# Performance work log

Measured on AMD Instinct MI355X. Metric: run time of the kernel, lower is better.

## Reference

```python
import jax, jax.numpy as jnp
import numpy as np

N, H, E, P = 100000, 64, 1600000, 3


def setup_inputs() -> dict:
    key = jax.random.key(0)
    ks = jax.random.split(key, 12)
    h = jax.random.normal(ks[0], (N, H), dtype=jnp.float32)
    W = jax.random.normal(ks[1], (P, H, H), dtype=jnp.float32) * 0.1
    b = jnp.zeros((P, H), dtype=jnp.float32)
    a = jnp.full((P,), 0.25, dtype=jnp.float32)  # PReLU slopes (torch default init)
    fc_w = jax.random.normal(ks[2], (H, H), dtype=jnp.float32) * 0.1
    fc_b = jnp.zeros((H,), dtype=jnp.float32)
    att = jax.random.normal(ks[3], (H,), dtype=jnp.float32) * 0.1
    adj_vals = jax.random.uniform(ks[4], (E,), dtype=jnp.float32) * (1.0 / 16.0)
    row = jax.random.randint(ks[5], (E,), 0, N, dtype=jnp.int32)
    col = jax.random.randint(ks[6], (E,), 0, N, dtype=jnp.int32)
    mask1 = jax.random.randint(ks[7], (N,), 0, 2, dtype=jnp.int32).astype(bool)
    mask2 = jax.random.randint(ks[8], (N,), 0, 2, dtype=jnp.int32).astype(bool)
    return {"h": h, "W": W, "b": b, "a": a, "fc_w": fc_w, "fc_b": fc_b,
            "att": att, "adj_vals": adj_vals, "row": row, "col": col,
            "mask1": mask1, "mask2": mask2}


def reference(h, W, b, a, fc_w, fc_b, att, adj_vals, row, col, mask1, mask2):
    n = h.shape[0]

    def gcn_all(x):
        # P GCN layers (small fixed P): linear -> spmm(adj) -> +bias -> PReLU
        outs = []
        for p in range(W.shape[0]):
            fts = x @ W[p].T                                   # [N,H]
            msg = fts[col] * adj_vals[:, None]                  # [E,H] gather
            agg = jax.ops.segment_sum(msg, row, num_segments=n) # [N,H] scatter-add
            o = agg + b[p]
            outs.append(jnp.where(o > 0, o, a[p] * o))          # PReLU
        return jnp.stack(outs)                                  # [P,N,H]

    def attention(embeds):
        # sp_p = mean_n tanh(fc(embed_p)); beta = softmax_p(att . sp_p)
        s = jnp.tanh(jnp.einsum('pnh,kh->pnk', embeds, fc_w) + fc_b).mean(axis=1)  # [P,H]
        beta = jax.nn.softmax(s @ att, axis=0)                                      # [P]
        return jnp.einsum('pnh,p->nh', embeds, beta)                                # [N,H]

    h_masked = h * (~mask1)[:, None].astype(h.dtype)
    z_mp = attention(gcn_all(h_masked))       # encode with mask_ratio1
    z_mp2 = attention(gcn_all(h))             # encode with mask_ratio 0
    z_masked = z_mp * (~mask2)[:, None].astype(h.dtype)
    x_recon = attention(gcn_all(z_masked))    # decode
    return (z_mp, z_mp2, x_recon)
```

## Files before the change

### kernel.cpp

```cpp
#include <hip/hip_runtime.h>
#include <hip/hip_bf16.h>

typedef __hip_bfloat16 bf16;
typedef __attribute__((ext_vector_type(8))) short bf16x8;
typedef __attribute__((ext_vector_type(4))) float f32x4;


__device__ __forceinline__ short f2bf(float x) {
    unsigned u = __float_as_uint(x);
    unsigned r = (u + 0x7FFFu + ((u >> 16) & 1u)) >> 16;
    return (short)r;
}
__device__ __forceinline__ float bf2f(short s) {
    return __uint_as_float(((unsigned)(unsigned short)s) << 16);
}

__device__ __forceinline__ void split8(const float* __restrict__ p, bool ok, bf16x8& hi,
                                       bf16x8& lo) {
    float v[8];
    if (ok) {
        float4 x0 = ((const float4*)p)[0];
        float4 x1 = ((const float4*)p)[1];
        v[0] = x0.x; v[1] = x0.y; v[2] = x0.z; v[3] = x0.w;
        v[4] = x1.x; v[5] = x1.y; v[6] = x1.z; v[7] = x1.w;
    } else {
#pragma unroll
        for (int j = 0; j < 8; j++) v[j] = 0.f;
    }
#pragma unroll
    for (int j = 0; j < 8; j++) {
        short hb = f2bf(v[j]);
        hi[j] = hb;
        lo[j] = f2bf(v[j] - bf2f(hb));
    }
}

__device__ __forceinline__ float fast_tanh(float x) {
    x = fminf(fmaxf(x, -15.f), 15.f);
    float t = __expf(2.f * x);
    return __fdividef(t - 1.f, t + 1.f);
}

__device__ __forceinline__ void fma4(float4& acc, float v, const float4& x) {
    acc.x = fmaf(v, x.x, acc.x);
    acc.y = fmaf(v, x.y, acc.y);
    acc.z = fmaf(v, x.z, acc.z);
    acc.w = fmaf(v, x.w, acc.w);
}

__device__ __forceinline__ void red4(float4& a) {
    a.x += __shfl_xor(a.x, 16); a.y += __shfl_xor(a.y, 16);
    a.z += __shfl_xor(a.z, 16); a.w += __shfl_xor(a.w, 16);
    a.x += __shfl_xor(a.x, 32); a.y += __shfl_xor(a.y, 32);
    a.z += __shfl_xor(a.z, 32); a.w += __shfl_xor(a.w, 32);
}

__global__ __launch_bounds__(256) void forensic_kernel(const unsigned int* __restrict__ mask_w,
                                                       const unsigned int* __restrict__ idx_w,
                                                       int nw_mask, int nw_idx,
                                                       int* __restrict__ flags) {
    __shared__ int sm[6];
    int t = threadIdx.x;
    if (t < 6) sm[t] = 0;
    __syncthreads();
    int m_gt1 = 0, m_f32 = 0, m_f64 = 0, m_oddnz = 0, i_hi = 0, i_oddnz = 0;
    for (int i = t; i < nw_mask; i += 256) {
        unsigned int w = mask_w[i];
        if (w > 1u && w != 0x3F800000u && w != 0x3FF00000u) m_gt1++;
        if (w == 0x3F800000u) m_f32++;
        if ((i & 1) && w == 0x3FF00000u) m_f64++;
        if ((i & 1) && w != 0u) m_oddnz++;
    }
    for (int i = t; i < nw_idx; i += 256) {
        unsigned int v = idx_w[i];
        if (v >= 0x20000000u) i_hi++;
        if ((i & 1) && v != 0u) i_oddnz++;
    }
    atomicAdd(&sm[0], m_gt1);
    atomicAdd(&sm[1], m_f32);
    atomicAdd(&sm[2], m_f64);
    atomicAdd(&sm[3], m_oddnz);
    atomicAdd(&sm[4], i_hi);
    atomicAdd(&sm[5], i_oddnz);
    __syncthreads();
    if (t == 0) {
        int mmode;
        if (sm[1] > 50) mmode = 2;
        else if (sm[2] > 50) mmode = 4;
        else if (sm[0] > 50) mmode = 0;
        else if (sm[3] > 50) mmode = 1;
        else mmode = 3;
        int imode;
        if (sm[4] > (nw_idx * 3) / 4) imode = 2;
        else if (sm[4] > nw_idx / 4) imode = 4;
        else if (sm[5] > 50) imode = 1;
        else imode = 3;
        flags[0] = mmode;
        flags[1] = imode;
    }
}

__device__ __forceinline__ int fetch_idx(const void* p, int e, int mode) {
    switch (mode) {
        case 1: return ((const int*)p)[e];
        case 3: return (int)(((const long long*)p)[e]);
        case 2: return (int)(((const float*)p)[e]);
        default: return (int)(((const double*)p)[e]);
    }
}

__global__ __launch_bounds__(256) void conv_mask_kernel(const void* __restrict__ m,
                                                        const int* __restrict__ flags, int n,
                                                        unsigned char* __restrict__ out) {
    int mode = flags[0];
    int i = blockIdx.x * 256 + threadIdx.x;
    if (i >= n) return;
    bool v;
    switch (mode) {
        case 0: v = ((const unsigned char*)m)[i] != 0; break;
        case 1: v = ((const int*)m)[i] != 0; break;
        case 2: v = ((const float*)m)[i] != 0.f; break;
        case 3: v = ((const long long*)m)[i] != 0; break;
        default: v = ((const double*)m)[i] != 0.0; break;
    }
    out[i] = v ? 1 : 0;
}


__global__ __launch_bounds__(256) void bucket_hist(const void* __restrict__ row,
                                                   const int* __restrict__ flags, int e_cnt,
                                                   int n, int shift, int nb,
                                                   int* __restrict__ bcnt) {
    __shared__ int hist[2048];
    int t = threadIdx.x;
    for (int i = t; i < nb; i += 256) hist[i] = 0;
    __syncthreads();
    int imode = flags[1];
    for (int e = blockIdx.x * 256 + t; e < e_cnt; e += gridDim.x * 256) {
        int r = fetch_idx(row, e, imode);
        if ((unsigned)r < (unsigned)n) atomicAdd(&hist[r >> shift], 1);
    }
    __syncthreads();
    for (int i = t; i < nb; i += 256)
        if (hist[i]) atomicAdd(&bcnt[i], hist[i]);
}

__global__ __launch_bounds__(1024) void bucket_scan(int* __restrict__ bptr, int nb,
                                                    int* __restrict__ bcur, int n,
                                                    int* __restrict__ row_ptr) {
    __shared__ int sh[1024];
    int t = threadIdx.x;
    int i0 = t * 2, i1 = t * 2 + 1;
    int a = (i0 < nb) ? bptr[i0] : 0;
    int b = (i1 < nb) ? bptr[i1] : 0;
    int s = a + b;
    sh[t] = s;
    __syncthreads();
    for (int off = 1; off < 1024; off <<= 1) {
        int u = (t >= off) ? sh[t - off] : 0;
        __syncthreads();
        sh[t] += u;
        __syncthreads();
    }
    int base = sh[t] - s;
    if (i0 < nb) { bptr[i0] = base; bcur[i0] = base; }
    if (i1 < nb) { bptr[i1] = base + a; bcur[i1] = base + a; }
    if (t == 1023) {
        bptr[nb] = sh[1023];
        row_ptr[n] = sh[1023];
    }
}

__global__ __launch_bounds__(256) void bin_pass2(const void* __restrict__ row,
                                                 const void* __restrict__ col,
                                                 const float* __restrict__ vals,
                                                 const int* __restrict__ flags, int e_cnt, int n,
                                                 int shift, int nb, int epb,
                                                 int* __restrict__ bcur,
                                                 int2* __restrict__ rcbin,
                                                 float* __restrict__ valbin) {
    __shared__ int hist[2048];
    __shared__ int base[2048];
    int t = threadIdx.x;
    int e0 = blockIdx.x * epb;
    int e1 = e0 + epb;
    if (e1 > e_cnt) e1 = e_cnt;
    if (e0 >= e_cnt) return;
    int imode = flags[1];
    for (int i = t; i < nb; i += 256) hist[i] = 0;
    __syncthreads();
    for (int e = e0 + t; e < e1; e += 256) {
        int r = fetch_idx(row, e, imode);
        if ((unsigned)r < (unsigned)n) atomicAdd(&hist[r >> shift], 1);
    }
    __syncthreads();
    for (int i = t; i < nb; i += 256) {
        int c = hist[i];
        base[i] = c ? atomicAdd(&bcur[i], c) : 0;
        hist[i] = 0;
    }
    __syncthreads();
    for (int e = e0 + t; e < e1; e += 256) {
        int r = fetch_idx(row, e, imode);
        if ((unsigned)r >= (unsigned)n) continue;
        int c = fetch_idx(col, e, imode);
        if ((unsigned)c >= (unsigned)n) c = 0;
        int bk = r >> shift;
        int pos = base[bk] + atomicAdd(&hist[bk], 1);
        rcbin[pos] = make_int2(r, c);
        valbin[pos] = vals[e];
    }
}

__global__ __launch_bounds__(256) void csr_finalize(const int* __restrict__ bptr,
                                                    const int2* __restrict__ rcbin,
                                                    const float* __restrict__ valbin, int n,
                                                    int shift, int* __restrict__ row_ptr,
                                                    int* __restrict__ col_s,
                                                    float* __restrict__ val_s) {
    __shared__ int cnt[1024];
    __shared__ int curs[1024];
    __shared__ int red[256];
    int b = blockIdx.x, t = threadIdx.x;
    int rpb = 1 << shift;
    int r0 = b << shift;
    int rows = n - r0;
    if (rows <= 0) return;
    if (rows > rpb) rows = rpb;
    int ebase = bptr[b], eend = bptr[b + 1];
    for (int i = t; i < rows; i += 256) cnt[i] = 0;
    __syncthreads();
    for (int e = ebase + t; e < eend; e += 256) atomicAdd(&cnt[rcbin[e].x - r0], 1);
    __syncthreads();
    int v[4], s = 0;
#pragma unroll
    for (int j = 0; j < 4; j++) {
        int idx = t * 4 + j;
        v[j] = (idx < rows) ? cnt[idx] : 0;
        s += v[j];
    }
    red[t] = s;
    __syncthreads();
    for (int off = 1; off < 256; off <<= 1) {
        int u = (t >= off) ? red[t - off] : 0;
        __syncthreads();
        red[t] += u;
        __syncthreads();
    }
    int run = ebase + red[t] - s;
#pragma unroll
    for (int j = 0; j < 4; j++) {
        int idx = t * 4 + j;
        if (idx < rows) {
            row_ptr[r0 + idx] = run;
            curs[idx] = run;
            run += v[j];
        }
    }
    __syncthreads();
    for (int e = ebase + t; e < eend; e += 256) {
        int2 rc = rcbin[e];
        float vv = valbin[e];
        int pos = atomicAdd(&curs[rc.x - r0], 1);
        col_s[pos] = rc.y;
        val_s[pos] = vv;
    }
}


__global__ __launch_bounds__(256) void spmm_dual(const float* __restrict__ X,
                                                 const int* __restrict__ row_ptr,
                                                 const int* __restrict__ col_s,
                                                 const float* __restrict__ val_s,
                                                 const unsigned char* __restrict__ mask, int n,
                                                 float* __restrict__ ax_m,
                                                 float* __restrict__ ax_f) {
    int gid = blockIdx.x * 256 + threadIdx.x;
    int r = gid >> 6;
    if (r >= n) return;
    int lane = threadIdx.x & 63;
    int g = lane >> 4, sub = lane & 15;
    int s = row_ptr[r], e = row_ptr[r + 1];
    int cnt = e - s;
    int myc = 0;
    float myvf = 0.f, myvm = 0.f;
    if (lane < cnt) {
        myc = col_s[s + lane];
        float v = val_s[s + lane];
        myvf = v;
        myvm = mask[myc] ? 0.f : v;
    }
    int cmain = cnt > 64 ? 64 : cnt;
    float4 fA = {0, 0, 0, 0}, fB = {0, 0, 0, 0}, mA = {0, 0, 0, 0}, mB = {0, 0, 0, 0};
    for (int i = 0; i < cmain; i += 8) {
        int iA = i + g, iB = i + 4 + g;
        int cA = __shfl(myc, iA), cB = __shfl(myc, iB);
        float vfA = __shfl(myvf, iA), vfB = __shfl(myvf, iB);
        float vmA = __shfl(myvm, iA), vmB = __shfl(myvm, iB);
        if (iA < cmain) {
            float4 x = *(const float4*)(X + (size_t)cA * 64 + sub * 4);
            fma4(fA, vfA, x);
            fma4(mA, vmA, x);
        }
        if (iB < cmain) {
            float4 x = *(const float4*)(X + (size_t)cB * 64 + sub * 4);
            fma4(fB, vfB, x);
            fma4(mB, vmB, x);
        }
    }
    for (int i = 64 + g; i < cnt; i += 4) {
        int c = col_s[s + i];
        float v = val_s[s + i];
        float vm = mask[c] ? 0.f : v;
        float4 x = *(const float4*)(X + (size_t)c * 64 + sub * 4);
        fma4(fA, v, x);
        fma4(mA, vm, x);
    }
    fA.x += fB.x; fA.y += fB.y; fA.z += fB.z; fA.w += fB.w;
    mA.x += mB.x; mA.y += mB.y; mA.z += mB.z; mA.w += mB.w;
    red4(fA);
    red4(mA);
    if (g == 0) {
        *(float4*)(ax_f + (size_t)r * 64 + sub * 4) = fA;
        *(float4*)(ax_m + (size_t)r * 64 + sub * 4) = mA;
    }
}

__global__ __launch_bounds__(256) void spmm_one(const float* __restrict__ X,
                                                const int* __restrict__ row_ptr,
                                                const int* __restrict__ col_s,
                                                const float* __restrict__ val_s,
                                                const unsigned char* __restrict__ mask, int n,
                                                float* __restrict__ ax) {
    int gid = blockIdx.x * 256 + threadIdx.x;
    int r = gid >> 6;
    if (r >= n) return;
    int lane = threadIdx.x & 63;
    int g = lane >> 4, sub = lane & 15;
    int s = row_ptr[r], e = row_ptr[r + 1];
    int cnt = e - s;
    int myc = 0;
    float myv = 0.f;
    if (lane < cnt) {
        myc = col_s[s + lane];
        float v = val_s[s + lane];
        myv = mask[myc] ? 0.f : v;
    }
    int cmain = cnt > 64 ? 64 : cnt;
    float4 aA = {0, 0, 0, 0}, aB = {0, 0, 0, 0};
    for (int i = 0; i < cmain; i += 8) {
        int iA = i + g, iB = i + 4 + g;
        int cA = __shfl(myc, iA), cB = __shfl(myc, iB);
        float vA = __shfl(myv, iA), vB = __shfl(myv, iB);
        if (iA < cmain && vA != 0.f) {
            float4 x = *(const float4*)(X + (size_t)cA * 64 + sub * 4);
            fma4(aA, vA, x);
        }
        if (iB < cmain && vB != 0.f) {
            float4 x = *(const float4*)(X + (size_t)cB * 64 + sub * 4);
            fma4(aB, vB, x);
        }
    }
    for (int i = 64 + g; i < cnt; i += 4) {
        int c = col_s[s + i];
        if (mask[c]) continue;
        float v = val_s[s + i];
        float4 x = *(const float4*)(X + (size_t)c * 64 + sub * 4);
        fma4(aA, v, x);
    }
    aA.x += aB.x; aA.y += aB.y; aA.z += aB.z; aA.w += aB.w;
    red4(aA);
    if (g == 0) *(float4*)(ax + (size_t)r * 64 + sub * 4) = aA;
}


template <int PP>
__global__ __launch_bounds__(256) void gemm_tanh(const float* __restrict__ X,
                                                 const float* __restrict__ Wg,
                                                 const float* __restrict__ b,
                                                 const float* __restrict__ a,
                                                 const float* __restrict__ fcw,
                                                 const float* __restrict__ fcb, int n,
                                                 float* __restrict__ s_sums) {
    __shared__ __align__(16) float tile[PP][16][68];
    int t = threadIdx.x;
    int wv = t >> 6, lane = t & 63, nl = lane & 15, q = lane >> 4;
    int colg = wv * 16 + nl;
    bf16x8 whi[PP][2], wlo[PP][2];
    float bias[PP], slope[PP];
#pragma unroll
    for (int p = 0; p < PP; p++) {
#pragma unroll
        for (int kk = 0; kk < 2; kk++)
            split8(Wg + p * 4096 + colg * 64 + kk * 32 + q * 8, true, whi[p][kk], wlo[p][kk]);
        bias[p] = b[p * 64 + colg];
        slope[p] = a[p];
    }
    bf16x8 fhi[2], flo[2];
#pragma unroll
    for (int kk = 0; kk < 2; kk++)
        split8(fcw + colg * 64 + kk * 32 + q * 8, true, fhi[kk], flo[kk]);
    float fbias = fcb[colg];
    float ssum[PP];
#pragma unroll
    for (int p = 0; p < PP; p++) ssum[p] = 0.f;

    int ntiles = (n + 15) >> 4;
    for (int rt = blockIdx.x; rt < ntiles; rt += gridDim.x) {
        int rowi = rt * 16 + nl;
        bool ok = rowi < n;
        bf16x8 ah[2], al[2];
#pragma unroll
        for (int kk = 0; kk < 2; kk++)
            split8(X + (size_t)rowi * 64 + kk * 32 + q * 8, ok, ah[kk], al[kk]);
#pragma unroll
        for (int p = 0; p < PP; p++) {
            f32x4 acc = {0.f, 0.f, 0.f, 0.f};
            acc = __builtin_amdgcn_mfma_f32_16x16x32_bf16(ah[0], whi[p][0], acc, 0, 0, 0);
            acc = __builtin_amdgcn_mfma_f32_16x16x32_bf16(ah[1], whi[p][1], acc, 0, 0, 0);
            acc = __builtin_amdgcn_mfma_f32_16x16x32_bf16(al[0], whi[p][0], acc, 0, 0, 0);
            acc = __builtin_amdgcn_mfma_f32_16x16x32_bf16(al[1], whi[p][1], acc, 0, 0, 0);
            acc = __builtin_amdgcn_mfma_f32_16x16x32_bf16(ah[0], wlo[p][0], acc, 0, 0, 0);
            acc = __builtin_amdgcn_mfma_f32_16x16x32_bf16(ah[1], wlo[p][1], acc, 0, 0, 0);
            acc = __builtin_amdgcn_mfma_f32_16x16x32_bf16(al[0], wlo[p][0], acc, 0, 0, 0);
            acc = __builtin_amdgcn_mfma_f32_16x16x32_bf16(al[1], wlo[p][1], acc, 0, 0, 0);
#pragma unroll
            for (int i = 0; i < 4; i++) {
                float o = acc[i] + bias[p];
                tile[p][q * 4 + i][colg] = (o > 0.f) ? o : slope[p] * o;
            }
        }
        __syncthreads();
#pragma unroll
        for (int p = 0; p < PP; p++) {
            bf16x8 eh[2], el[2];
#pragma unroll
            for (int kk = 0; kk < 2; kk++)
                split8(&tile[p][nl][kk * 32 + q * 8], true, eh[kk], el[kk]);
            f32x4 acc = {0.f, 0.f, 0.f, 0.f};
            acc = __builtin_amdgcn_mfma_f32_16x16x32_bf16(eh[0], fhi[0], acc, 0, 0, 0);
            acc = __builtin_amdgcn_mfma_f32_16x16x32_bf16(eh[1], fhi[1], acc, 0, 0, 0);
            acc = __builtin_amdgcn_mfma_f32_16x16x32_bf16(el[0], fhi[0], acc, 0, 0, 0);
            acc = __builtin_amdgcn_mfma_f32_16x16x32_bf16(el[1], fhi[1], acc, 0, 0, 0);
            acc = __builtin_amdgcn_mfma_f32_16x16x32_bf16(eh[0], flo[0], acc, 0, 0, 0);
            acc = __builtin_amdgcn_mfma_f32_16x16x32_bf16(eh[1], flo[1], acc, 0, 0, 0);
#pragma unroll
            for (int i = 0; i < 4; i++) {
                int r = rt * 16 + q * 4 + i;
                if (r < n) ssum[p] += fast_tanh(acc[i] + fbias);
            }
        }
        __syncthreads();
    }
#pragma unroll
    for (int p = 0; p < PP; p++) {
        float s = ssum[p];
        s += __shfl_xor(s, 16);
        s += __shfl_xor(s, 32);
        if (q == 0) atomicAdd(&s_sums[p * 64 + colg], s);
    }
}


template <int PP>
__global__ __launch_bounds__(256) void gemm_mix(const float* __restrict__ X,
                                                const float* __restrict__ Wg,
                                                const float* __restrict__ b,
                                                const float* __restrict__ a,
                                                const float* __restrict__ beta, int n,
                                                float* __restrict__ out, int accum) {
    int t = threadIdx.x;
    int wv = t >> 6, lane = t & 63, nl = lane & 15, q = lane >> 4;
    int colg = wv * 16 + nl;
    bf16x8 whi[PP][2], wlo[PP][2];
    float bias[PP], slope[PP], bet[PP];
#pragma unroll
    for (int p = 0; p < PP; p++) {
#pragma unroll
        for (int kk = 0; kk < 2; kk++)
            split8(Wg + p * 4096 + colg * 64 + kk * 32 + q * 8, true, whi[p][kk], wlo[p][kk]);
        bias[p] = b[p * 64 + colg];
        slope[p] = a[p];
        bet[p] = beta[p];
    }
    int ntiles = (n + 15) >> 4;
    for (int rt = blockIdx.x; rt < ntiles; rt += gridDim.x) {
        int rowi = rt * 16 + nl;
        bool ok = rowi < n;
        bf16x8 ah[2], al[2];
#pragma unroll
        for (int kk = 0; kk < 2; kk++)
            split8(X + (size_t)rowi * 64 + kk * 32 + q * 8, ok, ah[kk], al[kk]);
        float mix[4] = {0.f, 0.f, 0.f, 0.f};
#pragma unroll
        for (int p = 0; p < PP; p++) {
            f32x4 acc = {0.f, 0.f, 0.f, 0.f};
            acc = __builtin_amdgcn_mfma_f32_16x16x32_bf16(ah[0], whi[p][0], acc, 0, 0, 0);
            acc = __builtin_amdgcn_mfma_f32_16x16x32_bf16(ah[1], whi[p][1], acc, 0, 0, 0);
            acc = __builtin_amdgcn_mfma_f32_16x16x32_bf16(al[0], whi[p][0], acc, 0, 0, 0);
            acc = __builtin_amdgcn_mfma_f32_16x16x32_bf16(al[1], whi[p][1], acc, 0, 0, 0);
            acc = __builtin_amdgcn_mfma_f32_16x16x32_bf16(ah[0], wlo[p][0], acc, 0, 0, 0);
            acc = __builtin_amdgcn_mfma_f32_16x16x32_bf16(ah[1], wlo[p][1], acc, 0, 0, 0);
            acc = __builtin_amdgcn_mfma_f32_16x16x32_bf16(al[0], wlo[p][0], acc, 0, 0, 0);
            acc = __builtin_amdgcn_mfma_f32_16x16x32_bf16(al[1], wlo[p][1], acc, 0, 0, 0);
#pragma unroll
            for (int i = 0; i < 4; i++) {
                float o = acc[i] + bias[p];
                o = (o > 0.f) ? o : slope[p] * o;
                mix[i] = fmaf(bet[p], o, mix[i]);
            }
        }
#pragma unroll
        for (int i = 0; i < 4; i++) {
            int r = rt * 16 + q * 4 + i;
            if (r < n) {
                size_t idx = (size_t)r * 64 + colg;
                out[idx] = accum ? (out[idx] + mix[i]) : mix[i];
            }
        }
    }
}

__global__ __launch_bounds__(64) void compute_beta(const float* __restrict__ s_sums,
                                                   const float* __restrict__ att, int n, int P,
                                                   float* __restrict__ beta) {
    int lane = threadIdx.x;
    float av = att[lane];
    float l[8];
    for (int p = 0; p < P; p++) l[p] = s_sums[p * 64 + lane] * av;
#pragma unroll
    for (int off = 32; off > 0; off >>= 1)
        for (int p = 0; p < 8; p++)
            if (p < P) l[p] += __shfl_down(l[p], off);
    if (lane == 0) {
        const float inv = 1.0f / (float)n;
        float m = -1e30f;
        for (int p = 0; p < P; p++) {
            l[p] *= inv;
            m = fmaxf(m, l[p]);
        }
        float s = 0.f;
        for (int p = 0; p < P; p++) {
            l[p] = __expf(l[p] - m);
            s += l[p];
        }
        for (int p = 0; p < P; p++) beta[p] = l[p] / s;
    }
}


extern "C" void kernel_launch(void* const* d_in, const int* in_sizes, int n_in,
                              void* d_out, int out_size, void* d_ws, size_t ws_size,
                              hipStream_t stream) {
    const float* h = (const float*)d_in[0];
    const float* W = (const float*)d_in[1];
    const float* b = (const float*)d_in[2];
    const float* a = (const float*)d_in[3];
    const float* fc_w = (const float*)d_in[4];
    const float* fc_b = (const float*)d_in[5];
    const float* att = (const float*)d_in[6];
    const float* adj = (const float*)d_in[7];
    const void* row = d_in[8];
    const void* col = d_in[9];
    const void* mask1 = d_in[10];
    const void* mask2 = d_in[11];
    float* out = (float*)d_out;

    int P = in_sizes[3];
    if (P < 1 || P > 8) P = 3;
    int N = in_sizes[0] / 64;
    int E = in_sizes[7];

    int shift = 8;
    while (((N >> shift) + 1) > 2048) shift++;
    int NB = (N >> shift) + 1;

    char* w = (char*)d_ws;
    auto alloc = [&](size_t bytes) {
        void* p = (void*)w;
        w += (bytes + 255) & ~(size_t)255;
        return p;
    };
    int* row_ptr = (int*)alloc((size_t)(N + 1) * 4);
    int* col_s = (int*)alloc((size_t)E * 4);
    float* val_s = (float*)alloc((size_t)E * 4);
    int* bptr = (int*)alloc((size_t)(NB + 1) * 4);
    int* bcur = (int*)alloc((size_t)NB * 4);
    int2* rcbin = (int2*)alloc((size_t)E * 8);
    float* valbin = (float*)alloc((size_t)E * 4);
    unsigned char* m1c = (unsigned char*)alloc(N);
    unsigned char* m2c = (unsigned char*)alloc(N);
    float* axm = (float*)alloc((size_t)N * 64 * 4);
    float* axf = (float*)alloc((size_t)N * 64 * 4);
    float* s_sums = (float*)alloc(8 * 64 * 4);
    float* beta = (float*)alloc(8 * 4);
    int* flags = (int*)alloc(256);

    int nw_mask = N / 4 > 25000 ? 25000 : N / 4;
    int nw_idx = E / 4 > 25000 ? 25000 : E / 4;
    forensic_kernel<<<1, 256, 0, stream>>>((const unsigned int*)mask1, (const unsigned int*)row,
                                           nw_mask, nw_idx, flags);
    conv_mask_kernel<<<(N + 255) / 256, 256, 0, stream>>>(mask1, flags, N, m1c);
    conv_mask_kernel<<<(N + 255) / 256, 256, 0, stream>>>(mask2, flags, N, m2c);

    hipMemsetAsync(bptr, 0, (size_t)(NB + 1) * 4, stream);
    bucket_hist<<<1024, 256, 0, stream>>>(row, flags, E, N, shift, NB, bptr);
    bucket_scan<<<1, 1024, 0, stream>>>(bptr, NB, bcur, N, row_ptr);
    int epb = 8192;
    int bin_blocks = (E + epb - 1) / epb;
    bin_pass2<<<bin_blocks, 256, 0, stream>>>(row, col, adj, flags, E, N, shift, NB, epb, bcur,
                                              rcbin, valbin);
    csr_finalize<<<NB, 256, 0, stream>>>(bptr, rcbin, valbin, N, shift, row_ptr, col_s, val_s);

    int spmm_grid = ((size_t)N * 64 + 255) / 256;
    int gemm_blocks = 1024;

    auto tail = [&](const float* ax, float* dst) {
        hipMemsetAsync(s_sums, 0, 8 * 64 * 4, stream);
        if (P == 3) {
            gemm_tanh<3><<<gemm_blocks, 256, 0, stream>>>(ax, W, b, a, fc_w, fc_b, N, s_sums);
        } else {
            for (int p = 0; p < P; p++)
                gemm_tanh<1><<<gemm_blocks, 256, 0, stream>>>(ax, W + p * 4096, b + p * 64, a + p,
                                                              fc_w, fc_b, N, s_sums + p * 64);
        }
        compute_beta<<<1, 64, 0, stream>>>(s_sums, att, N, P, beta);
        if (P == 3) {
            gemm_mix<3><<<gemm_blocks, 256, 0, stream>>>(ax, W, b, a, beta, N, dst, 0);
        } else {
            for (int p = 0; p < P; p++)
                gemm_mix<1><<<gemm_blocks, 256, 0, stream>>>(ax, W + p * 4096, b + p * 64, a + p,
                                                             beta + p, N, dst, p != 0);
        }
    };

    spmm_dual<<<spmm_grid, 256, 0, stream>>>(h, row_ptr, col_s, val_s, m1c, N, axm, axf);
    tail(axm, out);
    tail(axf, out + (size_t)N * 64);
    spmm_one<<<spmm_grid, 256, 0, stream>>>(out, row_ptr, col_s, val_s, m2c, N, axm);
    tail(axm, out + (size_t)2 * N * 64);
}
```

Measured before the change: 655.7 us.

## Fuse mask conversion, register-cache bin pass, widen finalize and spmm unroll

Result: no change. 652.8 us (-0.4%).

```diff
diff --git a/kernel.cpp b/kernel.cpp
--- a/kernel.cpp
+++ b/kernel.cpp
@@ -109,21 +109,26 @@
     }
 }
 
-__global__ __launch_bounds__(256) void conv_mask_kernel(const void* __restrict__ m,
-                                                        const int* __restrict__ flags, int n,
-                                                        unsigned char* __restrict__ out) {
+__device__ __forceinline__ bool conv_one(const void* m, int mode, int i) {
+    switch (mode) {
+        case 0: return ((const unsigned char*)m)[i] != 0;
+        case 1: return ((const int*)m)[i] != 0;
+        case 2: return ((const float*)m)[i] != 0.f;
+        case 3: return ((const long long*)m)[i] != 0;
+        default: return ((const double*)m)[i] != 0.0;
+    }
+}
+
+__global__ __launch_bounds__(256) void conv_masks(const void* __restrict__ m1,
+                                                  const void* __restrict__ m2,
+                                                  const int* __restrict__ flags, int n,
+                                                  unsigned char* __restrict__ o1,
+                                                  unsigned char* __restrict__ o2) {
     int mode = flags[0];
     int i = blockIdx.x * 256 + threadIdx.x;
     if (i >= n) return;
-    bool v;
-    switch (mode) {
-        case 0: v = ((const unsigned char*)m)[i] != 0; break;
-        case 1: v = ((const int*)m)[i] != 0; break;
-        case 2: v = ((const float*)m)[i] != 0.f; break;
-        case 3: v = ((const long long*)m)[i] != 0; break;
-        default: v = ((const double*)m)[i] != 0.0; break;
-    }
-    out[i] = v ? 1 : 0;
+    o1[i] = conv_one(m1, mode, i) ? 1 : 0;
+    o2[i] = conv_one(m2, mode, i) ? 1 : 0;
 }
 
 
@@ -175,23 +180,35 @@
                                                  const void* __restrict__ col,
                                                  const float* __restrict__ vals,
                                                  const int* __restrict__ flags, int e_cnt, int n,
-                                                 int shift, int nb, int epb,
-                                                 int* __restrict__ bcur,
+                                                 int shift, int nb, int* __restrict__ bcur,
                                                  int2* __restrict__ rcbin,
                                                  float* __restrict__ valbin) {
     __shared__ int hist[2048];
     __shared__ int base[2048];
     int t = threadIdx.x;
-    int e0 = blockIdx.x * epb;
-    int e1 = e0 + epb;
-    if (e1 > e_cnt) e1 = e_cnt;
+    int e0 = blockIdx.x * 2048;
     if (e0 >= e_cnt) return;
     int imode = flags[1];
     for (int i = t; i < nb; i += 256) hist[i] = 0;
     __syncthreads();
-    for (int e = e0 + t; e < e1; e += 256) {
-        int r = fetch_idx(row, e, imode);
-        if ((unsigned)r < (unsigned)n) atomicAdd(&hist[r >> shift], 1);
+    int rr[8], cc[8];
+    float vv[8];
+    bool ok[8];
+#pragma unroll
+    for (int j = 0; j < 8; j++) {
+        int e = e0 + j * 256 + t;
+        ok[j] = false;
+        if (e < e_cnt) {
+            int r = fetch_idx(row, e, imode);
+            if ((unsigned)r < (unsigned)n) {
+                ok[j] = true;
+                rr[j] = r;
+                int c = fetch_idx(col, e, imode);
+                cc[j] = ((unsigned)c < (unsigned)n) ? c : 0;
+                vv[j] = vals[e];
+                atomicAdd(&hist[r >> shift], 1);
+            }
+        }
     }
     __syncthreads();
     for (int i = t; i < nb; i += 256) {
@@ -200,19 +217,18 @@
         hist[i] = 0;
     }
     __syncthreads();
-    for (int e = e0 + t; e < e1; e += 256) {
-        int r = fetch_idx(row, e, imode);
-        if ((unsigned)r >= (unsigned)n) continue;
-        int c = fetch_idx(col, e, imode);
-        if ((unsigned)c >= (unsigned)n) c = 0;
-        int bk = r >> shift;
-        int pos = base[bk] + atomicAdd(&hist[bk], 1);
-        rcbin[pos] = make_int2(r, c);
-        valbin[pos] = vals[e];
-    }
-}
-
-__global__ __launch_bounds__(256) void csr_finalize(const int* __restrict__ bptr,
+#pragma unroll
+    for (int j = 0; j < 8; j++) {
+        if (ok[j]) {
+            int bk = rr[j] >> shift;
+            int pos = base[bk] + atomicAdd(&hist[bk], 1);
+            rcbin[pos] = make_int2(rr[j], cc[j]);
+            valbin[pos] = vv[j];
+        }
+    }
+}
+
+__global__ __launch_bounds__(512) void csr_finalize(const int* __restrict__ bptr,
                                                     const int2* __restrict__ rcbin,
                                                     const float* __restrict__ valbin, int n,
                                                     int shift, int* __restrict__ row_ptr,
@@ -220,7 +236,7 @@
                                                     float* __restrict__ val_s) {
     __shared__ int cnt[1024];
     __shared__ int curs[1024];
-    __shared__ int red[256];
+    __shared__ int red[512];
     int b = blockIdx.x, t = threadIdx.x;
     int rpb = 1 << shift;
     int r0 = b << shift;
@@ -228,20 +244,20 @@
     if (rows <= 0) return;
     if (rows > rpb) rows = rpb;
     int ebase = bptr[b], eend = bptr[b + 1];
-    for (int i = t; i < rows; i += 256) cnt[i] = 0;
-    __syncthreads();
-    for (int e = ebase + t; e < eend; e += 256) atomicAdd(&cnt[rcbin[e].x - r0], 1);
-    __syncthreads();
-    int v[4], s = 0;
-#pragma unroll
-    for (int j = 0; j < 4; j++) {
-        int idx = t * 4 + j;
+    for (int i = t; i < rows; i += 512) cnt[i] = 0;
+    __syncthreads();
+    for (int e = ebase + t; e < eend; e += 512) atomicAdd(&cnt[rcbin[e].x - r0], 1);
+    __syncthreads();
+    int v[2], s = 0;
+#pragma unroll
+    for (int j = 0; j < 2; j++) {
+        int idx = t * 2 + j;
         v[j] = (idx < rows) ? cnt[idx] : 0;
         s += v[j];
     }
     red[t] = s;
     __syncthreads();
-    for (int off = 1; off < 256; off <<= 1) {
+    for (int off = 1; off < 512; off <<= 1) {
         int u = (t >= off) ? red[t - off] : 0;
         __syncthreads();
         red[t] += u;
@@ -249,8 +265,8 @@
     }
     int run = ebase + red[t] - s;
 #pragma unroll
-    for (int j = 0; j < 4; j++) {
-        int idx = t * 4 + j;
+    for (int j = 0; j < 2; j++) {
+        int idx = t * 2 + j;
         if (idx < rows) {
             row_ptr[r0 + idx] = run;
             curs[idx] = run;
@@ -258,7 +274,7 @@
         }
     }
     __syncthreads();
-    for (int e = ebase + t; e < eend; e += 256) {
+    for (int e = ebase + t; e < eend; e += 512) {
         int2 rc = rcbin[e];
         float vv = valbin[e];
         int pos = atomicAdd(&curs[rc.x - r0], 1);
@@ -292,20 +308,33 @@
     }
     int cmain = cnt > 64 ? 64 : cnt;
     float4 fA = {0, 0, 0, 0}, fB = {0, 0, 0, 0}, mA = {0, 0, 0, 0}, mB = {0, 0, 0, 0};
-    for (int i = 0; i < cmain; i += 8) {
-        int iA = i + g, iB = i + 4 + g;
-        int cA = __shfl(myc, iA), cB = __shfl(myc, iB);
-        float vfA = __shfl(myvf, iA), vfB = __shfl(myvf, iB);
-        float vmA = __shfl(myvm, iA), vmB = __shfl(myvm, iB);
-        if (iA < cmain) {
-            float4 x = *(const float4*)(X + (size_t)cA * 64 + sub * 4);
-            fma4(fA, vfA, x);
-            fma4(mA, vmA, x);
-        }
-        if (iB < cmain) {
-            float4 x = *(const float4*)(X + (size_t)cB * 64 + sub * 4);
-            fma4(fB, vfB, x);
-            fma4(mB, vmB, x);
+    for (int i = 0; i < cmain; i += 16) {
+        int i0 = i + g, i1 = i + 4 + g, i2 = i + 8 + g, i3 = i + 12 + g;
+        int c0 = __shfl(myc, i0), c1 = __shfl(myc, i1);
+        int c2 = __shfl(myc, i2), c3 = __shfl(myc, i3);
+        float vf0 = __shfl(myvf, i0), vf1 = __shfl(myvf, i1);
+        float vf2 = __shfl(myvf, i2), vf3 = __shfl(myvf, i3);
+        float vm0 = __shfl(myvm, i0), vm1 = __shfl(myvm, i1);
+        float vm2 = __shfl(myvm, i2), vm3 = __shfl(myvm, i3);
+        if (i0 < cmain) {
+            float4 x = *(const float4*)(X + (size_t)c0 * 64 + sub * 4);
+            fma4(fA, vf0, x);
+            fma4(mA, vm0, x);
+        }
+        if (i1 < cmain) {
+            float4 x = *(const float4*)(X + (size_t)c1 * 64 + sub * 4);
+            fma4(fB, vf1, x);
+            fma4(mB, vm1, x);
+        }
+        if (i2 < cmain) {
+            float4 x = *(const float4*)(X + (size_t)c2 * 64 + sub * 4);
+            fma4(fA, vf2, x);
+            fma4(mA, vm2, x);
+        }
+        if (i3 < cmain) {
+            float4 x = *(const float4*)(X + (size_t)c3 * 64 + sub * 4);
+            fma4(fB, vf3, x);
+            fma4(mB, vm3, x);
         }
     }
     for (int i = 64 + g; i < cnt; i += 4) {
@@ -348,17 +377,27 @@
     }
     int cmain = cnt > 64 ? 64 : cnt;
     float4 aA = {0, 0, 0, 0}, aB = {0, 0, 0, 0};
-    for (int i = 0; i < cmain; i += 8) {
-        int iA = i + g, iB = i + 4 + g;
-        int cA = __shfl(myc, iA), cB = __shfl(myc, iB);
-        float vA = __shfl(myv, iA), vB = __shfl(myv, iB);
-        if (iA < cmain && vA != 0.f) {
-            float4 x = *(const float4*)(X + (size_t)cA * 64 + sub * 4);
-            fma4(aA, vA, x);
-        }
-        if (iB < cmain && vB != 0.f) {
-            float4 x = *(const float4*)(X + (size_t)cB * 64 + sub * 4);
-            fma4(aB, vB, x);
+    for (int i = 0; i < cmain; i += 16) {
+        int i0 = i + g, i1 = i + 4 + g, i2 = i + 8 + g, i3 = i + 12 + g;
+        int c0 = __shfl(myc, i0), c1 = __shfl(myc, i1);
+        int c2 = __shfl(myc, i2), c3 = __shfl(myc, i3);
+        float v0 = __shfl(myv, i0), v1 = __shfl(myv, i1);
+        float v2 = __shfl(myv, i2), v3 = __shfl(myv, i3);
+        if (i0 < cmain && v0 != 0.f) {
+            float4 x = *(const float4*)(X + (size_t)c0 * 64 + sub * 4);
+            fma4(aA, v0, x);
+        }
+        if (i1 < cmain && v1 != 0.f) {
+            float4 x = *(const float4*)(X + (size_t)c1 * 64 + sub * 4);
+            fma4(aB, v1, x);
+        }
+        if (i2 < cmain && v2 != 0.f) {
+            float4 x = *(const float4*)(X + (size_t)c2 * 64 + sub * 4);
+            fma4(aA, v2, x);
+        }
+        if (i3 < cmain && v3 != 0.f) {
+            float4 x = *(const float4*)(X + (size_t)c3 * 64 + sub * 4);
+            fma4(aB, v3, x);
         }
     }
     for (int i = 64 + g; i < cnt; i += 4) {
@@ -600,20 +639,18 @@
     int nw_idx = E / 4 > 25000 ? 25000 : E / 4;
     forensic_kernel<<<1, 256, 0, stream>>>((const unsigned int*)mask1, (const unsigned int*)row,
                                            nw_mask, nw_idx, flags);
-    conv_mask_kernel<<<(N + 255) / 256, 256, 0, stream>>>(mask1, flags, N, m1c);
-    conv_mask_kernel<<<(N + 255) / 256, 256, 0, stream>>>(mask2, flags, N, m2c);
+    conv_masks<<<(N + 255) / 256, 256, 0, stream>>>(mask1, mask2, flags, N, m1c, m2c);
 
     hipMemsetAsync(bptr, 0, (size_t)(NB + 1) * 4, stream);
     bucket_hist<<<1024, 256, 0, stream>>>(row, flags, E, N, shift, NB, bptr);
     bucket_scan<<<1, 1024, 0, stream>>>(bptr, NB, bcur, N, row_ptr);
-    int epb = 8192;
-    int bin_blocks = (E + epb - 1) / epb;
-    bin_pass2<<<bin_blocks, 256, 0, stream>>>(row, col, adj, flags, E, N, shift, NB, epb, bcur,
-                                              rcbin, valbin);
-    csr_finalize<<<NB, 256, 0, stream>>>(bptr, rcbin, valbin, N, shift, row_ptr, col_s, val_s);
+    int bin_blocks = (E + 2047) / 2048;
+    bin_pass2<<<bin_blocks, 256, 0, stream>>>(row, col, adj, flags, E, N, shift, NB, bcur, rcbin,
+                                              valbin);
+    csr_finalize<<<NB, 512, 0, stream>>>(bptr, rcbin, valbin, N, shift, row_ptr, col_s, val_s);
 
     int spmm_grid = ((size_t)N * 64 + 255) / 256;
-    int gemm_blocks = 1024;
+    int gemm_blocks = 1536;
 
     auto tail = [&](const float* ax, float* dst) {
         hipMemsetAsync(s_sums, 0, 8 * 64 * 4, stream);
```
